# Kernel optimization log

Measured on AMD Instinct MI355X. Metric: run time of the kernel, lower is better.

## Reference

```python
import jax, jax.numpy as jnp
import numpy as np

D_S = 128
N_NODES = 50000
N_EDGES = 800000


def setup_inputs() -> dict:
    key = jax.random.key(0)
    k_s, k_e, k_w1, k_b1, k_w2, k_b2 = jax.random.split(key, 6)
    s = jax.random.normal(k_s, (N_NODES, D_S), dtype=jnp.float32)
    edge_index = jax.random.randint(k_e, (2, N_EDGES), 0, N_NODES, dtype=jnp.int64)
    # nn.Linear(2*d_s, d_s): W1 [d_s, 2*d_s], b1 [d_s]; nn.Linear(d_s, 1): W2 [1, d_s], b2 [1]
    lim1 = 1.0 / np.sqrt(2 * D_S)
    lim2 = 1.0 / np.sqrt(D_S)
    W1 = jax.random.uniform(k_w1, (D_S, 2 * D_S), jnp.float32, -lim1, lim1)
    b1 = jax.random.uniform(k_b1, (D_S,), jnp.float32, -lim1, lim1)
    W2 = jax.random.uniform(k_w2, (1, D_S), jnp.float32, -lim2, lim2)
    b2 = jax.random.uniform(k_b2, (1,), jnp.float32, -lim2, lim2)
    return {"s": s, "edge_index": edge_index, "W1": W1, "b1": b1, "W2": W2, "b2": b2}


def reference(s, edge_index, W1, b1, W2, b2):
    row, col = edge_index[0], edge_index[1]
    # Gather endpoint features and concat: h_edge [E, 2*d_s]
    h_edge = jnp.concatenate([s[row], s[col]], axis=-1)
    h = jax.nn.silu(h_edge @ W1.T + b1)          # [E, d_s]
    out = (h @ W2.T + b2).squeeze(-1)            # [E]
    return out
```

## Files before the change

### kernel.cpp

```cpp
#include <hip/hip_runtime.h>
#include <hip/hip_bf16.h>

#define D_S 128

typedef short bf16x8 __attribute__((ext_vector_type(8)));
typedef float f32x4 __attribute__((ext_vector_type(4)));

__device__ __forceinline__ unsigned short f32_to_bf16(float f) {
  unsigned int u = __float_as_uint(f);
  return (unsigned short)((u + 0x7FFFu + ((u >> 16) & 1u)) >> 16);
}
__device__ __forceinline__ unsigned int pack2_bf16(float lo, float hi) {
  return (unsigned int)f32_to_bf16(lo) | ((unsigned int)f32_to_bf16(hi) << 16);
}
__device__ __forceinline__ bf16x8 cvt_frag(float4 x, float4 y) {
  union { bf16x8 v; unsigned int u[4]; } r;
  r.u[0] = pack2_bf16(x.x, x.y);
  r.u[1] = pack2_bf16(x.z, x.w);
  r.u[2] = pack2_bf16(y.x, y.y);
  r.u[3] = pack2_bf16(y.z, y.w);
  return r.v;
}

__global__ __launch_bounds__(256, 1) void precompute_mfma(
    const float* __restrict__ s, const float* __restrict__ W1,
    const float* __restrict__ b1, unsigned short* __restrict__ AB,
    int n_nodes) {
  __shared__ __align__(16) unsigned short o_tile[64][136];
  int t = threadIdx.x;
  int wv = t >> 6, lane = t & 63;
  int lr = lane & 15, lc = lane >> 4;
  int n0 = blockIdx.x * 64;

  bf16x8 afrag[4][4];
#pragma unroll
  for (int m = 0; m < 4; ++m) {
    int r = n0 + m * 16 + lr;
    if (r > n_nodes - 1) r = n_nodes - 1;
    const float* ap = s + (size_t)r * D_S + lc * 8;
#pragma unroll
    for (int ks = 0; ks < 4; ++ks) {
      float4 x = *(const float4*)(ap + ks * 32);
      float4 y = *(const float4*)(ap + ks * 32 + 4);
      afrag[m][ks] = cvt_frag(x, y);
    }
  }

#pragma unroll 1
  for (int chunk = 0; chunk < 2; ++chunk) {
    f32x4 acc[4][2] = {};
    const float* wbase =
        W1 + (size_t)(wv * 32 + lr) * (2 * D_S) + chunk * D_S + lc * 8;
#pragma unroll
    for (int ks = 0; ks < 4; ++ks) {
      bf16x8 bfr[2];
#pragma unroll
      for (int nt = 0; nt < 2; ++nt) {
        const float* bp = wbase + (size_t)nt * 16 * (2 * D_S) + ks * 32;
        float4 x = *(const float4*)bp;
        float4 y = *(const float4*)(bp + 4);
        bfr[nt] = cvt_frag(x, y);
      }
#pragma unroll
      for (int m = 0; m < 4; ++m)
#pragma unroll
        for (int nt = 0; nt < 2; ++nt)
          acc[m][nt] = __builtin_amdgcn_mfma_f32_16x16x32_bf16(
              afrag[m][ks], bfr[nt], acc[m][nt], 0, 0, 0);
    }

    if (chunk == 0) {
#pragma unroll
      for (int nt = 0; nt < 2; ++nt) {
        float bv = b1[wv * 32 + nt * 16 + lr];
#pragma unroll
        for (int m = 0; m < 4; ++m)
#pragma unroll
          for (int r = 0; r < 4; ++r) acc[m][nt][r] += bv;
      }
    }

#pragma unroll
    for (int m = 0; m < 4; ++m)
#pragma unroll
      for (int nt = 0; nt < 2; ++nt) {
        int colc = wv * 32 + nt * 16 + lr;
#pragma unroll
        for (int r = 0; r < 4; ++r)
          o_tile[m * 16 + lc * 4 + r][colc] = f32_to_bf16(acc[m][nt][r]);
      }
    __syncthreads();
#pragma unroll
    for (int rep = 0; rep < 4; ++rep) {
      int idx = t + rep * 256;
      int rowi = idx >> 4, cg = (idx & 15) * 8;
      int gn = n0 + rowi;
      if (gn < n_nodes) {
        uint4 v = *(const uint4*)&o_tile[rowi][cg];
        *(uint4*)(AB + (size_t)gn * 256 + chunk * D_S + cg) = v;
      }
    }
    __syncthreads();
  }
}

__device__ __forceinline__ float silu2(unsigned int ua, unsigned int ub,
                                       float wlo, float whi) {
  float h0 = __uint_as_float(ua << 16) + __uint_as_float(ub << 16);
  float h1 = __uint_as_float(ua & 0xFFFF0000u) + __uint_as_float(ub & 0xFFFF0000u);
  float e0 = __builtin_amdgcn_exp2f(h0 * -1.442695041f);
  float e1 = __builtin_amdgcn_exp2f(h1 * -1.442695041f);
  float r0 = __builtin_amdgcn_rcpf(1.f + e0);
  float r1 = __builtin_amdgcn_rcpf(1.f + e1);
  return h0 * r0 * wlo + h1 * r1 * whi;
}

__global__ __launch_bounds__(256) void edge_kernel(
    const int* __restrict__ ei, const unsigned short* __restrict__ AB,
    const float* __restrict__ W2, const float* __restrict__ b2,
    float* __restrict__ out, int E) {
  int t = threadIdx.x;
  int wv = (blockIdx.x << 2) + (t >> 6);
  int lane = t & 63;
  int g = lane >> 3, sub = lane & 7;
  int e = wv * 8 + g;
  if (e >= E) e = E - 1;

  int row = ei[e];
  int col = ei[E + e];

  unsigned int offA = ((unsigned int)row << 8) + (sub << 4);
  unsigned int offB = ((unsigned int)col << 8) + 128 + (sub << 4);
  uint4 a0 = *(const uint4*)(AB + offA);
  uint4 a1 = *(const uint4*)(AB + offA + 8);
  uint4 b0 = *(const uint4*)(AB + offB);
  uint4 b1v = *(const uint4*)(AB + offB + 8);

  const float4* wp = (const float4*)(W2 + (sub << 4));
  float4 w0 = wp[0], w1 = wp[1], w2 = wp[2], w3 = wp[3];

  float p = 0.f;
  p += silu2(a0.x, b0.x, w0.x, w0.y);
  p += silu2(a0.y, b0.y, w0.z, w0.w);
  p += silu2(a0.z, b0.z, w1.x, w1.y);
  p += silu2(a0.w, b0.w, w1.z, w1.w);
  p += silu2(a1.x, b1v.x, w2.x, w2.y);
  p += silu2(a1.y, b1v.y, w2.z, w2.w);
  p += silu2(a1.z, b1v.z, w3.x, w3.y);
  p += silu2(a1.w, b1v.w, w3.z, w3.w);

#pragma unroll
  for (int off = 1; off < 8; off <<= 1) p += __shfl_xor(p, off, 64);

  if (sub == 0) out[e] = p + b2[0];
}

__global__ __launch_bounds__(256) void edge_direct(
    const float* __restrict__ s, const int* __restrict__ ei,
    const float* __restrict__ W1, const float* __restrict__ b1,
    const float* __restrict__ W2, const float* __restrict__ b2,
    float* __restrict__ out, int E) {
  __shared__ float sh[256];
  __shared__ float red[128];
  int e = blockIdx.x;
  int t = threadIdx.x;
  int row = ei[e], col = ei[E + e];
  sh[t] = (t < 128) ? s[(size_t)row * D_S + t] : s[(size_t)col * D_S + (t - 128)];
  __syncthreads();
  if (t < 128) {
    float acc = b1[t];
    const float* w = W1 + (size_t)t * 256;
#pragma unroll 8
    for (int jj = 0; jj < 256; ++jj) acc += sh[jj] * w[jj];
    red[t] = (acc / (1.f + __expf(-acc))) * W2[t];
  }
  __syncthreads();
  if (t < 64) {
    float x = red[t] + red[t + 64];
#pragma unroll
    for (int off = 32; off; off >>= 1) x += __shfl_xor(x, off, 64);
    if (t == 0) out[e] = x + b2[0];
  }
}

extern "C" void kernel_launch(void* const* d_in, const int* in_sizes, int n_in,
                              void* d_out, int out_size, void* d_ws, size_t ws_size,
                              hipStream_t stream) {
  const float* s  = (const float*)d_in[0];
  const int*   ei = (const int*)d_in[1];
  const float* W1 = (const float*)d_in[2];
  const float* b1 = (const float*)d_in[3];
  const float* W2 = (const float*)d_in[4];
  const float* b2 = (const float*)d_in[5];
  float* out = (float*)d_out;

  int n_nodes = in_sizes[0] / D_S;
  int E = in_sizes[1] / 2;

  size_t need = (size_t)n_nodes * 256 * sizeof(unsigned short);
  if (ws_size >= need) {
    unsigned short* AB = (unsigned short*)d_ws;
    precompute_mfma<<<(n_nodes + 63) / 64, 256, 0, stream>>>(s, W1, b1, AB, n_nodes);
    int blocks = (E + 31) / 32;
    edge_kernel<<<blocks, 256, 0, stream>>>(ei, AB, W2, b2, out, E);
  } else {
    edge_direct<<<E, 256, 0, stream>>>(s, ei, W1, b1, W2, b2, out, E);
  }
}
```

Before: 89.45 us.

## Pre-convert W1 to bf16, split precompute by chunk, process two edges per lane-group

```diff
diff --git a/kernel.cpp b/kernel.cpp
--- a/kernel.cpp
+++ b/kernel.cpp
@@ -22,8 +22,20 @@
   return r.v;
 }
 
-__global__ __launch_bounds__(256, 1) void precompute_mfma(
-    const float* __restrict__ s, const float* __restrict__ W1,
+__global__ __launch_bounds__(256) void w1_to_bf16(
+    const float* __restrict__ W1, unsigned short* __restrict__ W1bf) {
+  int idx4 = (blockIdx.x * 256 + threadIdx.x) * 4;
+  int j = idx4 >> 7, k = idx4 & 127;
+  const float* src =
+      W1 + ((j < D_S) ? (size_t)j * (2 * D_S) + k : (size_t)(j - D_S) * (2 * D_S) + D_S + k);
+  float4 v = *(const float4*)src;
+  ushort4 o = make_ushort4(f32_to_bf16(v.x), f32_to_bf16(v.y),
+                           f32_to_bf16(v.z), f32_to_bf16(v.w));
+  *(ushort4*)(W1bf + idx4) = o;
+}
+
+__global__ __launch_bounds__(256) void precompute_mfma(
+    const float* __restrict__ s, const unsigned short* __restrict__ W1bf,
     const float* __restrict__ b1, unsigned short* __restrict__ AB,
     int n_nodes) {
   __shared__ __align__(16) unsigned short o_tile[64][136];
@@ -31,6 +43,18 @@
   int wv = t >> 6, lane = t & 63;
   int lr = lane & 15, lc = lane >> 4;
   int n0 = blockIdx.x * 64;
+  int chunk = blockIdx.y;
+
+  bf16x8 bfr[2][4];
+  {
+    const unsigned short* wb =
+        W1bf + (size_t)(chunk * 128 + wv * 32 + lr) * D_S + lc * 8;
+#pragma unroll
+    for (int nt = 0; nt < 2; ++nt)
+#pragma unroll
+      for (int ks = 0; ks < 4; ++ks)
+        bfr[nt][ks] = *(const bf16x8*)(wb + nt * 16 * D_S + ks * 32);
+  }
 
   bf16x8 afrag[4][4];
 #pragma unroll
@@ -46,61 +70,46 @@
     }
   }
 
-#pragma unroll 1
-  for (int chunk = 0; chunk < 2; ++chunk) {
-    f32x4 acc[4][2] = {};
-    const float* wbase =
-        W1 + (size_t)(wv * 32 + lr) * (2 * D_S) + chunk * D_S + lc * 8;
-#pragma unroll
-    for (int ks = 0; ks < 4; ++ks) {
-      bf16x8 bfr[2];
-#pragma unroll
-      for (int nt = 0; nt < 2; ++nt) {
-        const float* bp = wbase + (size_t)nt * 16 * (2 * D_S) + ks * 32;
-        float4 x = *(const float4*)bp;
-        float4 y = *(const float4*)(bp + 4);
-        bfr[nt] = cvt_frag(x, y);
-      }
+  f32x4 acc[4][2] = {};
+#pragma unroll
+  for (int ks = 0; ks < 4; ++ks)
+#pragma unroll
+    for (int m = 0; m < 4; ++m)
+#pragma unroll
+      for (int nt = 0; nt < 2; ++nt)
+        acc[m][nt] = __builtin_amdgcn_mfma_f32_16x16x32_bf16(
+            afrag[m][ks], bfr[nt][ks], acc[m][nt], 0, 0, 0);
+
+  if (chunk == 0) {
+#pragma unroll
+    for (int nt = 0; nt < 2; ++nt) {
+      float bv = b1[wv * 32 + nt * 16 + lr];
 #pragma unroll
       for (int m = 0; m < 4; ++m)
 #pragma unroll
-        for (int nt = 0; nt < 2; ++nt)
-          acc[m][nt] = __builtin_amdgcn_mfma_f32_16x16x32_bf16(
-              afrag[m][ks], bfr[nt], acc[m][nt], 0, 0, 0);
-    }
-
-    if (chunk == 0) {
-#pragma unroll
-      for (int nt = 0; nt < 2; ++nt) {
-        float bv = b1[wv * 32 + nt * 16 + lr];
-#pragma unroll
-        for (int m = 0; m < 4; ++m)
-#pragma unroll
-          for (int r = 0; r < 4; ++r) acc[m][nt][r] += bv;
-      }
-    }
-
-#pragma unroll
-    for (int m = 0; m < 4; ++m)
-#pragma unroll
-      for (int nt = 0; nt < 2; ++nt) {
-        int colc = wv * 32 + nt * 16 + lr;
-#pragma unroll
-        for (int r = 0; r < 4; ++r)
-          o_tile[m * 16 + lc * 4 + r][colc] = f32_to_bf16(acc[m][nt][r]);
-      }
-    __syncthreads();
-#pragma unroll
-    for (int rep = 0; rep < 4; ++rep) {
-      int idx = t + rep * 256;
-      int rowi = idx >> 4, cg = (idx & 15) * 8;
-      int gn = n0 + rowi;
-      if (gn < n_nodes) {
-        uint4 v = *(const uint4*)&o_tile[rowi][cg];
-        *(uint4*)(AB + (size_t)gn * 256 + chunk * D_S + cg) = v;
-      }
-    }
-    __syncthreads();
+        for (int r = 0; r < 4; ++r) acc[m][nt][r] += bv;
+    }
+  }
+
+#pragma unroll
+  for (int m = 0; m < 4; ++m)
+#pragma unroll
+    for (int nt = 0; nt < 2; ++nt) {
+      int colc = wv * 32 + nt * 16 + lr;
+#pragma unroll
+      for (int r = 0; r < 4; ++r)
+        o_tile[m * 16 + lc * 4 + r][colc] = f32_to_bf16(acc[m][nt][r]);
+    }
+  __syncthreads();
+#pragma unroll
+  for (int rep = 0; rep < 4; ++rep) {
+    int idx = t + rep * 256;
+    int rowi = idx >> 4, cg = (idx & 15) * 8;
+    int gn = n0 + rowi;
+    if (gn < n_nodes) {
+      uint4 v = *(const uint4*)&o_tile[rowi][cg];
+      *(uint4*)(AB + (size_t)gn * 256 + chunk * D_S + cg) = v;
+    }
   }
 }
 
@@ -115,30 +124,9 @@
   return h0 * r0 * wlo + h1 * r1 * whi;
 }
 
-__global__ __launch_bounds__(256) void edge_kernel(
-    const int* __restrict__ ei, const unsigned short* __restrict__ AB,
-    const float* __restrict__ W2, const float* __restrict__ b2,
-    float* __restrict__ out, int E) {
-  int t = threadIdx.x;
-  int wv = (blockIdx.x << 2) + (t >> 6);
-  int lane = t & 63;
-  int g = lane >> 3, sub = lane & 7;
-  int e = wv * 8 + g;
-  if (e >= E) e = E - 1;
-
-  int row = ei[e];
-  int col = ei[E + e];
-
-  unsigned int offA = ((unsigned int)row << 8) + (sub << 4);
-  unsigned int offB = ((unsigned int)col << 8) + 128 + (sub << 4);
-  uint4 a0 = *(const uint4*)(AB + offA);
-  uint4 a1 = *(const uint4*)(AB + offA + 8);
-  uint4 b0 = *(const uint4*)(AB + offB);
-  uint4 b1v = *(const uint4*)(AB + offB + 8);
-
-  const float4* wp = (const float4*)(W2 + (sub << 4));
-  float4 w0 = wp[0], w1 = wp[1], w2 = wp[2], w3 = wp[3];
-
+__device__ __forceinline__ float silu_dot16(uint4 a0, uint4 a1, uint4 b0,
+                                            uint4 b1v, float4 w0, float4 w1,
+                                            float4 w2, float4 w3) {
   float p = 0.f;
   p += silu2(a0.x, b0.x, w0.x, w0.y);
   p += silu2(a0.y, b0.y, w0.z, w0.w);
@@ -148,11 +136,54 @@
   p += silu2(a1.y, b1v.y, w2.z, w2.w);
   p += silu2(a1.z, b1v.z, w3.x, w3.y);
   p += silu2(a1.w, b1v.w, w3.z, w3.w);
-
-#pragma unroll
-  for (int off = 1; off < 8; off <<= 1) p += __shfl_xor(p, off, 64);
-
-  if (sub == 0) out[e] = p + b2[0];
+  return p;
+}
+
+__global__ __launch_bounds__(256) void edge_kernel(
+    const int* __restrict__ ei, const unsigned short* __restrict__ AB,
+    const float* __restrict__ W2, const float* __restrict__ b2,
+    float* __restrict__ out, int E) {
+  int t = threadIdx.x;
+  int wv = (blockIdx.x << 2) + (t >> 6);
+  int lane = t & 63;
+  int g = lane >> 3, sub = lane & 7;
+  int e0 = wv * 16 + (g << 1);
+  if (e0 > E - 2) e0 = E - 2;
+
+  int2 rr = *(const int2*)(ei + e0);
+  int2 cc = *(const int2*)(ei + E + e0);
+
+  unsigned int sh = (unsigned int)(sub << 4);
+  unsigned int offA0 = ((unsigned int)rr.x << 8) + sh;
+  unsigned int offA1 = ((unsigned int)rr.y << 8) + sh;
+  unsigned int offB0 = ((unsigned int)cc.x << 8) + 128 + sh;
+  unsigned int offB1 = ((unsigned int)cc.y << 8) + 128 + sh;
+
+  uint4 a00 = *(const uint4*)(AB + offA0);
+  uint4 a01 = *(const uint4*)(AB + offA0 + 8);
+  uint4 b00 = *(const uint4*)(AB + offB0);
+  uint4 b01 = *(const uint4*)(AB + offB0 + 8);
+  uint4 a10 = *(const uint4*)(AB + offA1);
+  uint4 a11 = *(const uint4*)(AB + offA1 + 8);
+  uint4 b10 = *(const uint4*)(AB + offB1);
+  uint4 b11 = *(const uint4*)(AB + offB1 + 8);
+
+  const float4* wp = (const float4*)(W2 + (sub << 4));
+  float4 w0 = wp[0], w1 = wp[1], w2 = wp[2], w3 = wp[3];
+
+  float p0 = silu_dot16(a00, a01, b00, b01, w0, w1, w2, w3);
+  float p1 = silu_dot16(a10, a11, b10, b11, w0, w1, w2, w3);
+
+#pragma unroll
+  for (int off = 1; off < 8; off <<= 1) {
+    p0 += __shfl_xor(p0, off, 64);
+    p1 += __shfl_xor(p1, off, 64);
+  }
+
+  if (sub == 0) {
+    float bb = b2[0];
+    *(float2*)(out + e0) = make_float2(p0 + bb, p1 + bb);
+  }
 }
 
 __global__ __launch_bounds__(256) void edge_direct(
@@ -197,11 +228,15 @@
   int n_nodes = in_sizes[0] / D_S;
   int E = in_sizes[1] / 2;
 
-  size_t need = (size_t)n_nodes * 256 * sizeof(unsigned short);
-  if (ws_size >= need) {
+  size_t ab_elems = (size_t)n_nodes * 256;
+  size_t need = (ab_elems + 65536) * sizeof(unsigned short);
+  if (ws_size >= need && E >= 2) {
     unsigned short* AB = (unsigned short*)d_ws;
-    precompute_mfma<<<(n_nodes + 63) / 64, 256, 0, stream>>>(s, W1, b1, AB, n_nodes);
-    int blocks = (E + 31) / 32;
+    unsigned short* W1bf = AB + ab_elems;
+    w1_to_bf16<<<64, 256, 0, stream>>>(W1, W1bf);
+    dim3 g1((n_nodes + 63) / 64, 2);
+    precompute_mfma<<<g1, 256, 0, stream>>>(s, W1bf, b1, AB, n_nodes);
+    int blocks = (E + 63) / 64;
     edge_kernel<<<blocks, 256, 0, stream>>>(ei, AB, W2, b2, out, E);
   } else {
     edge_direct<<<E, 256, 0, stream>>>(s, ei, W1, b1, W2, b2, out, E);
```

New measurement: 96.16 us. +7.5%, slower.

## Slice node tables by feature so each L2 cache holds one slice

Applied to the files above, without the earlier changes.

```diff
diff --git a/kernel.cpp b/kernel.cpp
--- a/kernel.cpp
+++ b/kernel.cpp
@@ -22,52 +22,69 @@
   return r.v;
 }
 
-__global__ __launch_bounds__(256, 1) void precompute_mfma(
+__global__ __launch_bounds__(256) void precompute_mfma(
     const float* __restrict__ s, const float* __restrict__ W1,
-    const float* __restrict__ b1, unsigned short* __restrict__ AB,
-    int n_nodes) {
-  __shared__ __align__(16) unsigned short o_tile[64][136];
+    const float* __restrict__ b1, unsigned short* __restrict__ Atab,
+    unsigned short* __restrict__ Btab, int n_nodes) {
+  __shared__ __align__(16) unsigned short s_tile[64 * 128];
+  __shared__ __align__(16) unsigned short o_tile[64 * 256];
   int t = threadIdx.x;
   int wv = t >> 6, lane = t & 63;
   int lr = lane & 15, lc = lane >> 4;
   int n0 = blockIdx.x * 64;
 
+#pragma unroll
+  for (int rep = 0; rep < 4; ++rep) {
+    int idx = t + rep * 256;
+    int row = idx >> 4;
+    int c8 = (idx & 15) * 8;
+    int gn = n0 + row;
+    if (gn > n_nodes - 1) gn = n_nodes - 1;
+    const float* sp = s + (size_t)gn * D_S + c8;
+    float4 x = *(const float4*)sp;
+    float4 y = *(const float4*)(sp + 4);
+    bf16x8 pk = cvt_frag(x, y);
+    int byte = (row * 256 + c8 * 2) ^ ((row & 7) << 4);
+    *(bf16x8*)((char*)s_tile + byte) = pk;
+  }
+  __syncthreads();
+
   bf16x8 afrag[4][4];
 #pragma unroll
   for (int m = 0; m < 4; ++m) {
-    int r = n0 + m * 16 + lr;
-    if (r > n_nodes - 1) r = n_nodes - 1;
-    const float* ap = s + (size_t)r * D_S + lc * 8;
+    int row = m * 16 + lr;
+    int swz = (row & 7) << 4;
 #pragma unroll
     for (int ks = 0; ks < 4; ++ks) {
-      float4 x = *(const float4*)(ap + ks * 32);
-      float4 y = *(const float4*)(ap + ks * 32 + 4);
-      afrag[m][ks] = cvt_frag(x, y);
+      int byte = (row * 256 + lc * 16 + ks * 64) ^ swz;
+      afrag[m][ks] = *(const bf16x8*)((const char*)s_tile + byte);
     }
   }
 
 #pragma unroll 1
   for (int chunk = 0; chunk < 2; ++chunk) {
+    bf16x8 bfr[2][4];
+#pragma unroll
+    for (int nt = 0; nt < 2; ++nt) {
+      const float* wrow =
+          W1 + (size_t)(wv * 32 + nt * 16 + lr) * (2 * D_S) + chunk * D_S + lc * 8;
+#pragma unroll
+      for (int ks = 0; ks < 4; ++ks) {
+        float4 x = *(const float4*)(wrow + ks * 32);
+        float4 y = *(const float4*)(wrow + ks * 32 + 4);
+        bfr[nt][ks] = cvt_frag(x, y);
+      }
+    }
+
     f32x4 acc[4][2] = {};
-    const float* wbase =
-        W1 + (size_t)(wv * 32 + lr) * (2 * D_S) + chunk * D_S + lc * 8;
-#pragma unroll
-    for (int ks = 0; ks < 4; ++ks) {
-      bf16x8 bfr[2];
-#pragma unroll
-      for (int nt = 0; nt < 2; ++nt) {
-        const float* bp = wbase + (size_t)nt * 16 * (2 * D_S) + ks * 32;
-        float4 x = *(const float4*)bp;
-        float4 y = *(const float4*)(bp + 4);
-        bfr[nt] = cvt_frag(x, y);
-      }
+#pragma unroll
+    for (int ks = 0; ks < 4; ++ks)
 #pragma unroll
       for (int m = 0; m < 4; ++m)
 #pragma unroll
         for (int nt = 0; nt < 2; ++nt)
           acc[m][nt] = __builtin_amdgcn_mfma_f32_16x16x32_bf16(
-              afrag[m][ks], bfr[nt], acc[m][nt], 0, 0, 0);
-    }
+              afrag[m][ks], bfr[nt][ks], acc[m][nt], 0, 0, 0);
 
     if (chunk == 0) {
 #pragma unroll
@@ -84,23 +101,35 @@
     for (int m = 0; m < 4; ++m)
 #pragma unroll
       for (int nt = 0; nt < 2; ++nt) {
-        int colc = wv * 32 + nt * 16 + lr;
-#pragma unroll
-        for (int r = 0; r < 4; ++r)
-          o_tile[m * 16 + lc * 4 + r][colc] = f32_to_bf16(acc[m][nt][r]);
+        int col = chunk * 128 + wv * 32 + nt * 16 + lr;
+#pragma unroll
+        for (int r = 0; r < 4; ++r) {
+          int row = m * 16 + lc * 4 + r;
+          int byte = (row * 512 + col * 2) ^ ((row & 7) << 4);
+          *(unsigned short*)((char*)o_tile + byte) = f32_to_bf16(acc[m][nt][r]);
+        }
       }
-    __syncthreads();
-#pragma unroll
-    for (int rep = 0; rep < 4; ++rep) {
-      int idx = t + rep * 256;
-      int rowi = idx >> 4, cg = (idx & 15) * 8;
-      int gn = n0 + rowi;
-      if (gn < n_nodes) {
-        uint4 v = *(const uint4*)&o_tile[rowi][cg];
-        *(uint4*)(AB + (size_t)gn * 256 + chunk * D_S + cg) = v;
-      }
-    }
-    __syncthreads();
+  }
+  __syncthreads();
+
+#pragma unroll
+  for (int rep = 0; rep < 2; ++rep) {
+    int idx = t + rep * 256;
+    int sl = idx >> 6, node = idx & 63;
+    int gn = n0 + node;
+    if (gn < n_nodes) {
+      int sw = (node & 7) << 4;
+      int base = node * 512 + sl * 32;
+      uint4 ra0 = *(const uint4*)((const char*)o_tile + ((base) ^ sw));
+      uint4 ra1 = *(const uint4*)((const char*)o_tile + ((base + 16) ^ sw));
+      uint4 rb0 = *(const uint4*)((const char*)o_tile + ((base + 256) ^ sw));
+      uint4 rb1 = *(const uint4*)((const char*)o_tile + ((base + 256 + 16) ^ sw));
+      size_t rec = ((size_t)sl * n_nodes + gn) << 4;
+      *(uint4*)(Atab + rec) = ra0;
+      *(uint4*)(Atab + rec + 8) = ra1;
+      *(uint4*)(Btab + rec) = rb0;
+      *(uint4*)(Btab + rec + 8) = rb1;
+    }
   }
 }
 
@@ -115,44 +144,47 @@
   return h0 * r0 * wlo + h1 * r1 * whi;
 }
 
-__global__ __launch_bounds__(256) void edge_kernel(
-    const int* __restrict__ ei, const unsigned short* __restrict__ AB,
-    const float* __restrict__ W2, const float* __restrict__ b2,
+__global__ __launch_bounds__(256) void edge_sliced(
+    const int* __restrict__ ei, const unsigned short* __restrict__ Atab,
+    const unsigned short* __restrict__ Btab, const float* __restrict__ W2,
+    float* __restrict__ P, int E, int N) {
+  int bid = blockIdx.x;
+  int slice = bid & 7;
+  int e = (bid >> 3) * 256 + threadIdx.x;
+  if (e >= E) return;
+
+  int row = __builtin_nontemporal_load(ei + e);
+  int col = __builtin_nontemporal_load(ei + E + e);
+
+  const uint4* pa = (const uint4*)(Atab + (((size_t)slice * N + row) << 4));
+  const uint4* pb = (const uint4*)(Btab + (((size_t)slice * N + col) << 4));
+  uint4 a0 = pa[0], a1 = pa[1];
+  uint4 b0 = pb[0], b1v = pb[1];
+
+  const float* w = W2 + (slice << 4);
+  float p = 0.f;
+  p += silu2(a0.x, b0.x, w[0], w[1]);
+  p += silu2(a0.y, b0.y, w[2], w[3]);
+  p += silu2(a0.z, b0.z, w[4], w[5]);
+  p += silu2(a0.w, b0.w, w[6], w[7]);
+  p += silu2(a1.x, b1v.x, w[8], w[9]);
+  p += silu2(a1.y, b1v.y, w[10], w[11]);
+  p += silu2(a1.z, b1v.z, w[12], w[13]);
+  p += silu2(a1.w, b1v.w, w[14], w[15]);
+
+  __builtin_nontemporal_store(p, P + (size_t)slice * E + e);
+}
+
+__global__ __launch_bounds__(256) void combine(
+    const float* __restrict__ P, const float* __restrict__ b2,
     float* __restrict__ out, int E) {
-  int t = threadIdx.x;
-  int wv = (blockIdx.x << 2) + (t >> 6);
-  int lane = t & 63;
-  int g = lane >> 3, sub = lane & 7;
-  int e = wv * 8 + g;
-  if (e >= E) e = E - 1;
-
-  int row = ei[e];
-  int col = ei[E + e];
-
-  unsigned int offA = ((unsigned int)row << 8) + (sub << 4);
-  unsigned int offB = ((unsigned int)col << 8) + 128 + (sub << 4);
-  uint4 a0 = *(const uint4*)(AB + offA);
-  uint4 a1 = *(const uint4*)(AB + offA + 8);
-  uint4 b0 = *(const uint4*)(AB + offB);
-  uint4 b1v = *(const uint4*)(AB + offB + 8);
-
-  const float4* wp = (const float4*)(W2 + (sub << 4));
-  float4 w0 = wp[0], w1 = wp[1], w2 = wp[2], w3 = wp[3];
-
-  float p = 0.f;
-  p += silu2(a0.x, b0.x, w0.x, w0.y);
-  p += silu2(a0.y, b0.y, w0.z, w0.w);
-  p += silu2(a0.z, b0.z, w1.x, w1.y);
-  p += silu2(a0.w, b0.w, w1.z, w1.w);
-  p += silu2(a1.x, b1v.x, w2.x, w2.y);
-  p += silu2(a1.y, b1v.y, w2.z, w2.w);
-  p += silu2(a1.z, b1v.z, w3.x, w3.y);
-  p += silu2(a1.w, b1v.w, w3.z, w3.w);
-
-#pragma unroll
-  for (int off = 1; off < 8; off <<= 1) p += __shfl_xor(p, off, 64);
-
-  if (sub == 0) out[e] = p + b2[0];
+  int e = blockIdx.x * 256 + threadIdx.x;
+  if (e >= E) return;
+  float v = b2[0];
+#pragma unroll
+  for (int k = 0; k < 8; ++k)
+    v += __builtin_nontemporal_load(P + (size_t)k * E + e);
+  out[e] = v;
 }
 
 __global__ __launch_bounds__(256) void edge_direct(
@@ -197,12 +229,19 @@
   int n_nodes = in_sizes[0] / D_S;
   int E = in_sizes[1] / 2;
 
-  size_t need = (size_t)n_nodes * 256 * sizeof(unsigned short);
+  size_t tab_elems = (size_t)8 * n_nodes * 16;
+  size_t need = 2 * tab_elems * sizeof(unsigned short) +
+                (size_t)8 * E * sizeof(float);
   if (ws_size >= need) {
-    unsigned short* AB = (unsigned short*)d_ws;
-    precompute_mfma<<<(n_nodes + 63) / 64, 256, 0, stream>>>(s, W1, b1, AB, n_nodes);
-    int blocks = (E + 31) / 32;
-    edge_kernel<<<blocks, 256, 0, stream>>>(ei, AB, W2, b2, out, E);
+    unsigned short* Atab = (unsigned short*)d_ws;
+    unsigned short* Btab = Atab + tab_elems;
+    float* P = (float*)(Btab + tab_elems);
+    precompute_mfma<<<(n_nodes + 63) / 64, 256, 0, stream>>>(s, W1, b1, Atab,
+                                                             Btab, n_nodes);
+    int nchunk = (E + 255) / 256;
+    edge_sliced<<<nchunk * 8, 256, 0, stream>>>(ei, Atab, Btab, W2, P, E,
+                                                n_nodes);
+    combine<<<nchunk, 256, 0, stream>>>(P, b2, out, E);
   } else {
     edge_direct<<<E, 256, 0, stream>>>(s, ei, W1, b1, W2, b2, out, E);
   }
```

New measurement: 103.1 us. 15.3% more time.

## Stage node features through swizzled LDS and write full output rows once

Applied to the files above, without the earlier changes.

```diff
diff --git a/kernel.cpp b/kernel.cpp
--- a/kernel.cpp
+++ b/kernel.cpp
@@ -22,52 +22,69 @@
   return r.v;
 }
 
-__global__ __launch_bounds__(256, 1) void precompute_mfma(
+__global__ __launch_bounds__(256) void precompute_mfma(
     const float* __restrict__ s, const float* __restrict__ W1,
     const float* __restrict__ b1, unsigned short* __restrict__ AB,
     int n_nodes) {
-  __shared__ __align__(16) unsigned short o_tile[64][136];
+  __shared__ __align__(16) unsigned short s_tile[64 * 128];
+  __shared__ __align__(16) unsigned short o_tile[64 * 256];
   int t = threadIdx.x;
   int wv = t >> 6, lane = t & 63;
   int lr = lane & 15, lc = lane >> 4;
   int n0 = blockIdx.x * 64;
 
+#pragma unroll
+  for (int rep = 0; rep < 4; ++rep) {
+    int idx = t + rep * 256;
+    int row = idx >> 4;
+    int c8 = (idx & 15) * 8;
+    int gn = n0 + row;
+    if (gn > n_nodes - 1) gn = n_nodes - 1;
+    const float* sp = s + (size_t)gn * D_S + c8;
+    float4 x = *(const float4*)sp;
+    float4 y = *(const float4*)(sp + 4);
+    bf16x8 pk = cvt_frag(x, y);
+    int byte = (row * 256 + c8 * 2) ^ ((row & 7) << 4);
+    *(bf16x8*)((char*)s_tile + byte) = pk;
+  }
+  __syncthreads();
+
   bf16x8 afrag[4][4];
 #pragma unroll
   for (int m = 0; m < 4; ++m) {
-    int r = n0 + m * 16 + lr;
-    if (r > n_nodes - 1) r = n_nodes - 1;
-    const float* ap = s + (size_t)r * D_S + lc * 8;
+    int row = m * 16 + lr;
+    int swz = (row & 7) << 4;
 #pragma unroll
     for (int ks = 0; ks < 4; ++ks) {
-      float4 x = *(const float4*)(ap + ks * 32);
-      float4 y = *(const float4*)(ap + ks * 32 + 4);
-      afrag[m][ks] = cvt_frag(x, y);
+      int byte = (row * 256 + lc * 16 + ks * 64) ^ swz;
+      afrag[m][ks] = *(const bf16x8*)((const char*)s_tile + byte);
     }
   }
 
 #pragma unroll 1
   for (int chunk = 0; chunk < 2; ++chunk) {
+    bf16x8 bfr[2][4];
+#pragma unroll
+    for (int nt = 0; nt < 2; ++nt) {
+      const float* wrow =
+          W1 + (size_t)(wv * 32 + nt * 16 + lr) * (2 * D_S) + chunk * D_S + lc * 8;
+#pragma unroll
+      for (int ks = 0; ks < 4; ++ks) {
+        float4 x = *(const float4*)(wrow + ks * 32);
+        float4 y = *(const float4*)(wrow + ks * 32 + 4);
+        bfr[nt][ks] = cvt_frag(x, y);
+      }
+    }
+
     f32x4 acc[4][2] = {};
-    const float* wbase =
-        W1 + (size_t)(wv * 32 + lr) * (2 * D_S) + chunk * D_S + lc * 8;
-#pragma unroll
-    for (int ks = 0; ks < 4; ++ks) {
-      bf16x8 bfr[2];
-#pragma unroll
-      for (int nt = 0; nt < 2; ++nt) {
-        const float* bp = wbase + (size_t)nt * 16 * (2 * D_S) + ks * 32;
-        float4 x = *(const float4*)bp;
-        float4 y = *(const float4*)(bp + 4);
-        bfr[nt] = cvt_frag(x, y);
-      }
+#pragma unroll
+    for (int ks = 0; ks < 4; ++ks)
 #pragma unroll
       for (int m = 0; m < 4; ++m)
 #pragma unroll
         for (int nt = 0; nt < 2; ++nt)
           acc[m][nt] = __builtin_amdgcn_mfma_f32_16x16x32_bf16(
-              afrag[m][ks], bfr[nt], acc[m][nt], 0, 0, 0);
-    }
+              afrag[m][ks], bfr[nt][ks], acc[m][nt], 0, 0, 0);
 
     if (chunk == 0) {
 #pragma unroll
@@ -84,23 +101,31 @@
     for (int m = 0; m < 4; ++m)
 #pragma unroll
       for (int nt = 0; nt < 2; ++nt) {
-        int colc = wv * 32 + nt * 16 + lr;
-#pragma unroll
-        for (int r = 0; r < 4; ++r)
-          o_tile[m * 16 + lc * 4 + r][colc] = f32_to_bf16(acc[m][nt][r]);
+        int col = chunk * 128 + wv * 32 + nt * 16 + lr;
+#pragma unroll
+        for (int r = 0; r < 4; ++r) {
+          int row = m * 16 + lc * 4 + r;
+          int byte = (row * 512 + col * 2) ^ ((row & 7) << 4);
+          *(unsigned short*)((char*)o_tile + byte) = f32_to_bf16(acc[m][nt][r]);
+        }
       }
-    __syncthreads();
-#pragma unroll
-    for (int rep = 0; rep < 4; ++rep) {
-      int idx = t + rep * 256;
-      int rowi = idx >> 4, cg = (idx & 15) * 8;
-      int gn = n0 + rowi;
-      if (gn < n_nodes) {
-        uint4 v = *(const uint4*)&o_tile[rowi][cg];
-        *(uint4*)(AB + (size_t)gn * 256 + chunk * D_S + cg) = v;
-      }
-    }
-    __syncthreads();
+  }
+  __syncthreads();
+
+#pragma unroll
+  for (int rep = 0; rep < 4; ++rep) {
+    int idx = t + rep * 256;
+    int node = idx >> 4, jg = idx & 15;
+    int gn = n0 + node;
+    if (gn < n_nodes) {
+      int sw = (node & 7) << 4;
+      int base = node * 512 + jg * 32;
+      uint4 v0 = *(const uint4*)((const char*)o_tile + (base ^ sw));
+      uint4 v1 = *(const uint4*)((const char*)o_tile + ((base + 16) ^ sw));
+      unsigned short* dst = AB + (size_t)gn * 256 + jg * 16;
+      *(uint4*)dst = v0;
+      *(uint4*)(dst + 8) = v1;
+    }
   }
 }
 
@@ -129,8 +154,9 @@
   int row = ei[e];
   int col = ei[E + e];
 
-  unsigned int offA = ((unsigned int)row << 8) + (sub << 4);
-  unsigned int offB = ((unsigned int)col << 8) + 128 + (sub << 4);
+  unsigned int sh = (unsigned int)(sub << 4);
+  unsigned int offA = ((unsigned int)row << 8) + sh;
+  unsigned int offB = ((unsigned int)col << 8) + 128 + sh;
   uint4 a0 = *(const uint4*)(AB + offA);
   uint4 a1 = *(const uint4*)(AB + offA + 8);
   uint4 b0 = *(const uint4*)(AB + offB);
@@ -200,7 +226,8 @@
   size_t need = (size_t)n_nodes * 256 * sizeof(unsigned short);
   if (ws_size >= need) {
     unsigned short* AB = (unsigned short*)d_ws;
-    precompute_mfma<<<(n_nodes + 63) / 64, 256, 0, stream>>>(s, W1, b1, AB, n_nodes);
+    precompute_mfma<<<(n_nodes + 63) / 64, 256, 0, stream>>>(s, W1, b1, AB,
+                                                             n_nodes);
     int blocks = (E + 31) / 32;
     edge_kernel<<<blocks, 256, 0, stream>>>(ei, AB, W2, b2, out, E);
   } else {
```

Measured after the change: 81.90 us. 8.4% less time.
